# Performance work log

Measured on AMD Instinct MI355X. Metric: run time of the kernel, lower is better.

## Reference

```python
import jax, jax.numpy as jnp
import numpy as np

N_NODES = 50000
N_EDGES = 600000
D_IN = 128
D_HID = 128
D_OUT = 128
LN_EPS = 1e-5


def _layer_norm(h, g, b):
    mu = jnp.mean(h, axis=-1, keepdims=True)
    var = jnp.var(h, axis=-1, keepdims=True)
    return (h - mu) * jax.lax.rsqrt(var + LN_EPS) * g + b


def _gin_conv(x, src, dst, w1, b1, w2, b2):
    # sum-aggregate neighbor messages at destination nodes, eps = 0
    agg = jax.ops.segment_sum(x[src], dst, num_segments=x.shape[0])
    h = x + agg
    h = jax.nn.relu(h @ w1 + b1)
    return h @ w2 + b2


def setup_inputs() -> dict:
    key = jax.random.key(0)
    ks = jax.random.split(key, 20)
    x = jax.random.normal(ks[0], (N_NODES, D_IN), dtype=jnp.float32)
    edge_index = jax.random.randint(ks[1], (2, N_EDGES), 0, N_NODES, dtype=jnp.int64)
    dims = [(D_IN, D_HID), (D_HID, D_HID), (D_HID, D_HID), (D_HID, D_OUT)]
    inp = {"x": x, "edge_index": edge_index}
    for i, (din, dout) in enumerate(dims):
        s1 = 1.0 / np.sqrt(din)
        s2 = 1.0 / np.sqrt(D_HID)
        inp[f"w1_{i}"] = jax.random.uniform(ks[2 + 4 * i], (din, D_HID), jnp.float32, -s1, s1)
        inp[f"b1_{i}"] = jax.random.uniform(ks[3 + 4 * i], (D_HID,), jnp.float32, -s1, s1)
        inp[f"w2_{i}"] = jax.random.uniform(ks[4 + 4 * i], (D_HID, dout), jnp.float32, -s2, s2)
        inp[f"b2_{i}"] = jax.random.uniform(ks[5 + 4 * i], (dout,), jnp.float32, -s2, s2)
    for i in range(3):  # LayerNorm only on first 3 blocks
        inp[f"g_{i}"] = jnp.ones((D_HID,), jnp.float32)
        inp[f"beta_{i}"] = jnp.zeros((D_HID,), jnp.float32)
    return inp


def reference(x, edge_index,
              w1_0, b1_0, w2_0, b2_0,
              w1_1, b1_1, w2_1, b2_1,
              w1_2, b1_2, w2_2, b2_2,
              w1_3, b1_3, w2_3, b2_3,
              g_0, beta_0, g_1, beta_1, g_2, beta_2):
    src, dst = edge_index[0], edge_index[1]
    mlps = [(w1_0, b1_0, w2_0, b2_0), (w1_1, b1_1, w2_1, b2_1),
            (w1_2, b1_2, w2_2, b2_2), (w1_3, b1_3, w2_3, b2_3)]
    lns = [(g_0, beta_0), (g_1, beta_1), (g_2, beta_2)]
    h = x
    for i in range(3):
        h = _gin_conv(h, src, dst, *mlps[i])
        h = _layer_norm(h, *lns[i])
        h = jax.nn.relu(h)  # dropout rate 0.0 -> identity
    h = _gin_conv(h, src, dst, *mlps[3])  # final block: no norm/act
    return h
```

## Files before the change

### kernel.cpp

```cpp
#include <hip/hip_runtime.h>
#include <hip/hip_bf16.h>

#define NN 50000
#define NE 600000
#define DD 128
#define LDSW 136
#define NB 196
#define BSH 8
#define BSTR 4096
#define EPB 2048
#define NBLK_AC ((NE + EPB - 1) / EPB)

typedef __bf16 bf16;
typedef __attribute__((ext_vector_type(8))) __bf16 bf16x8;
typedef __attribute__((ext_vector_type(4))) float f32x4;
typedef __attribute__((ext_vector_type(4))) unsigned int u32x4;
typedef __attribute__((ext_vector_type(4))) unsigned short u16x4;
typedef unsigned short u16;

__device__ __forceinline__ float bf_lo(unsigned int u) {
    return __builtin_bit_cast(float, u << 16);
}
__device__ __forceinline__ float bf_hi(unsigned int u) {
    return __builtin_bit_cast(float, u & 0xffff0000u);
}
__device__ __forceinline__ unsigned int bf_pack(float x, float y) {
    u16 a = __builtin_bit_cast(u16, (bf16)x);
    u16 b = __builtin_bit_cast(u16, (bf16)y);
    return (unsigned int)a | ((unsigned int)b << 16);
}

struct Ptr8 { const float* p[8]; };

__device__ __forceinline__ int edge_dst(const int* ei, int e, int f) {
    return f ? ei[2 * NE + 2 * e] : ei[NE + e];
}
__device__ __forceinline__ int edge_src(const int* ei, int e, int f) {
    return f ? ei[2 * e] : ei[e];
}

#define J1 (NN * DD / 4)
#define J2 (J1 + 8 * DD * DD)

__global__ __launch_bounds__(256) void k_init(const float* __restrict__ x,
                                              u16* __restrict__ xb,
                                              Ptr8 ws, u16* __restrict__ wt,
                                              int* __restrict__ bcnt,
                                              const int* __restrict__ ei,
                                              int* __restrict__ flag) {
    int tid = threadIdx.x;
    if (blockIdx.x == 0) {
        if (tid == 0) flag[0] = 1;
        __syncthreads();
        if (ei[2 * tid + 1] != 0) flag[0] = 0;
    }
    int id = blockIdx.x * 256 + tid;
    if (id < NB) bcnt[id] = 0;
    if (id < J1) {
        f32x4 v = *(const f32x4*)(x + (size_t)id * 4);
        u16x4 o;
        o.x = __builtin_bit_cast(u16, (bf16)v.x);
        o.y = __builtin_bit_cast(u16, (bf16)v.y);
        o.z = __builtin_bit_cast(u16, (bf16)v.z);
        o.w = __builtin_bit_cast(u16, (bf16)v.w);
        *(u16x4*)(xb + (size_t)id * 4) = o;
    } else if (id < J2) {
        int i = id - J1;
        int m = i >> 14;
        int rem = i & 16383;
        int k = rem >> 7;
        int n = rem & 127;
        bf16 b = (bf16)ws.p[m][k * DD + n];
        wt[(size_t)m * DD * DD + n * DD + k] = __builtin_bit_cast(u16, b);
    }
}

__global__ __launch_bounds__(256) void k_scatter(const int* __restrict__ ei,
                                                 const int* __restrict__ flag,
                                                 int* __restrict__ bcnt,
                                                 unsigned int* __restrict__ tmp) {
    __shared__ int lh[NB];
    __shared__ int gb[NB];
    int tid = threadIdx.x;
    if (tid < NB) lh[tid] = 0;
    __syncthreads();
    int f = flag[0];
    int src[8], dst[8], lp[8];
    bool val[8];
#pragma unroll
    for (int k = 0; k < 8; k++) {
        int e = blockIdx.x * EPB + k * 256 + tid;
        val[k] = (e < NE);
        if (val[k]) {
            src[k] = edge_src(ei, e, f);
            dst[k] = edge_dst(ei, e, f);
            lp[k] = atomicAdd(&lh[dst[k] >> BSH], 1);
        }
    }
    __syncthreads();
    if (tid < NB && lh[tid] > 0) gb[tid] = atomicAdd(&bcnt[tid], lh[tid]);
    __syncthreads();
#pragma unroll
    for (int k = 0; k < 8; k++) {
        if (val[k]) {
            int bkt = dst[k] >> BSH;
            unsigned int pk = (unsigned)src[k] | ((unsigned)(dst[k] & 255) << 16);
            tmp[(size_t)bkt * BSTR + gb[bkt] + lp[k]] = pk;
        }
    }
}

__global__ __launch_bounds__(256) void k_build(const unsigned int* __restrict__ tmp,
                                               const int* __restrict__ bcnt,
                                               int* __restrict__ row_start,
                                               int* __restrict__ adj) {
    __shared__ int cnt[256];
    __shared__ int ccur[256];
    __shared__ int sm[4];
    int b = blockIdx.x, tid = threadIdx.x;
    int base = b << BSH;
    int lane = tid & 63, w = tid >> 6;
    cnt[tid] = 0;
    int v = (tid < b) ? bcnt[tid] : 0;
#pragma unroll
    for (int off = 1; off < 64; off <<= 1) v += __shfl_xor(v, off);
    if (lane == 0) sm[w] = v;
    __syncthreads();
    int G = sm[0] + sm[1] + sm[2] + sm[3];
    int n = bcnt[b];
    size_t ts = (size_t)b * BSTR;
    for (int i = tid; i < n; i += 256) {
        atomicAdd(&cnt[tmp[ts + i] >> 16], 1);
    }
    __syncthreads();
    int v2 = cnt[tid];
    int orig = v2;
#pragma unroll
    for (int off = 1; off < 64; off <<= 1) {
        int t = __shfl_up(v2, off);
        if (lane >= off) v2 += t;
    }
    if (lane == 63) sm[w] = v2;
    __syncthreads();
    int add = 0;
    for (int k = 0; k < w; k++) add += sm[k];
    int ex = G + (v2 - orig) + add;
    ccur[tid] = ex;
    if (base + tid < NN) row_start[base + tid] = ex;
    if (b == 0 && tid == 0) row_start[NN] = NE;
    __syncthreads();
    for (int i = tid; i < n; i += 256) {
        unsigned int pk = tmp[ts + i];
        int p = atomicAdd(&ccur[pk >> 16], 1);
        adj[p] = (int)(pk & 0xffffu);
    }
}

__global__ __launch_bounds__(256) void k_agg(const u16* __restrict__ xb,
                                             const int* __restrict__ row_start,
                                             const int* __restrict__ adj,
                                             u16* __restrict__ out) {
    int gid = blockIdx.x * blockDim.x + threadIdx.x;
    int wave = gid >> 6, lane = gid & 63;
    int grp = lane >> 4, l = lane & 15;
    int node = wave * 4 + grp;
    if (node >= NN) return;
    const u32x4* base = (const u32x4*)xb;
    u32x4 sv = base[(size_t)node * 16 + l];
    float af[8], bf[8];
#pragma unroll
    for (int j = 0; j < 4; j++) {
        af[2 * j] = bf_lo(sv[j]); af[2 * j + 1] = bf_hi(sv[j]);
        bf[2 * j] = 0.f; bf[2 * j + 1] = 0.f;
    }
    int s = row_start[node], e = row_start[node + 1];
    int i = s;
    for (; i + 7 < e; i += 8) {
        u32x4 t0 = base[(size_t)adj[i] * 16 + l];
        u32x4 t1 = base[(size_t)adj[i + 1] * 16 + l];
        u32x4 t2 = base[(size_t)adj[i + 2] * 16 + l];
        u32x4 t3 = base[(size_t)adj[i + 3] * 16 + l];
        u32x4 t4 = base[(size_t)adj[i + 4] * 16 + l];
        u32x4 t5 = base[(size_t)adj[i + 5] * 16 + l];
        u32x4 t6 = base[(size_t)adj[i + 6] * 16 + l];
        u32x4 t7 = base[(size_t)adj[i + 7] * 16 + l];
#pragma unroll
        for (int j = 0; j < 4; j++) {
            af[2 * j]     += (bf_lo(t0[j]) + bf_lo(t1[j])) + (bf_lo(t2[j]) + bf_lo(t3[j]));
            af[2 * j + 1] += (bf_hi(t0[j]) + bf_hi(t1[j])) + (bf_hi(t2[j]) + bf_hi(t3[j]));
            bf[2 * j]     += (bf_lo(t4[j]) + bf_lo(t5[j])) + (bf_lo(t6[j]) + bf_lo(t7[j]));
            bf[2 * j + 1] += (bf_hi(t4[j]) + bf_hi(t5[j])) + (bf_hi(t6[j]) + bf_hi(t7[j]));
        }
    }
    for (; i + 3 < e; i += 4) {
        u32x4 t0 = base[(size_t)adj[i] * 16 + l];
        u32x4 t1 = base[(size_t)adj[i + 1] * 16 + l];
        u32x4 t2 = base[(size_t)adj[i + 2] * 16 + l];
        u32x4 t3 = base[(size_t)adj[i + 3] * 16 + l];
#pragma unroll
        for (int j = 0; j < 4; j++) {
            af[2 * j]     += bf_lo(t0[j]) + bf_lo(t1[j]);
            af[2 * j + 1] += bf_hi(t0[j]) + bf_hi(t1[j]);
            bf[2 * j]     += bf_lo(t2[j]) + bf_lo(t3[j]);
            bf[2 * j + 1] += bf_hi(t2[j]) + bf_hi(t3[j]);
        }
    }
    for (; i < e; i++) {
        u32x4 t = base[(size_t)adj[i] * 16 + l];
#pragma unroll
        for (int j = 0; j < 4; j++) { af[2 * j] += bf_lo(t[j]); af[2 * j + 1] += bf_hi(t[j]); }
    }
    u32x4 o;
#pragma unroll
    for (int j = 0; j < 4; j++) o[j] = bf_pack(af[2 * j] + bf[2 * j], af[2 * j + 1] + bf[2 * j + 1]);
    ((u32x4*)out)[(size_t)node * 16 + l] = o;
}

template <bool LN, bool B16OUT>
__global__ __launch_bounds__(64) void k_mlp(const u16* __restrict__ hin,
                                            const u16* __restrict__ w1t,
                                            const float* __restrict__ b1,
                                            const u16* __restrict__ w2t,
                                            const float* __restrict__ b2,
                                            const float* __restrict__ g,
                                            const float* __restrict__ bta,
                                            void* __restrict__ hout) {
    __shared__ u16 lds[64 * LDSW];
    const int lane = threadIdx.x;
    const int l15 = lane & 15, l4 = lane >> 4;
    const int tile0 = blockIdx.x * 64;

#pragma unroll
    for (int it = 0; it < 16; ++it) {
        int slot = lane + it * 64;
        int row = slot >> 4, c16 = slot & 15;
        u32x4 v = {0u, 0u, 0u, 0u};
        int grow = tile0 + row;
        if (grow < NN) v = *(const u32x4*)(hin + (size_t)grow * DD + c16 * 8);
        *(u32x4*)&lds[row * LDSW + c16 * 8] = v;
    }
    __syncthreads();

    float b1c[8], b2c[8], gc[8], bc[8];
#pragma unroll
    for (int c = 0; c < 8; c++) {
        int col = c * 16 + l15;
        b1c[c] = b1[col];
        b2c[c] = b2[col];
        if (LN) { gc[c] = g[col]; bc[c] = bta[col]; }
    }

    f32x4 acc[4][8];
#pragma unroll
    for (int r = 0; r < 4; r++)
#pragma unroll
        for (int c = 0; c < 8; c++) acc[r][c] = (f32x4){0.f, 0.f, 0.f, 0.f};

#pragma unroll
    for (int ks = 0; ks < 4; ++ks) {
        bf16x8 a0 = __builtin_bit_cast(bf16x8,
            *(const u32x4*)&lds[(l15) * LDSW + ks * 32 + l4 * 8]);
        bf16x8 a1 = __builtin_bit_cast(bf16x8,
            *(const u32x4*)&lds[(16 + l15) * LDSW + ks * 32 + l4 * 8]);
        bf16x8 a2 = __builtin_bit_cast(bf16x8,
            *(const u32x4*)&lds[(32 + l15) * LDSW + ks * 32 + l4 * 8]);
        bf16x8 a3 = __builtin_bit_cast(bf16x8,
            *(const u32x4*)&lds[(48 + l15) * LDSW + ks * 32 + l4 * 8]);
#pragma unroll
        for (int c = 0; c < 8; c++) {
            bf16x8 b = __builtin_bit_cast(bf16x8,
                *(const u32x4*)(w1t + (size_t)(c * 16 + l15) * DD + ks * 32 + l4 * 8));
            acc[0][c] = __builtin_amdgcn_mfma_f32_16x16x32_bf16(a0, b, acc[0][c], 0, 0, 0);
            acc[1][c] = __builtin_amdgcn_mfma_f32_16x16x32_bf16(a1, b, acc[1][c], 0, 0, 0);
            acc[2][c] = __builtin_amdgcn_mfma_f32_16x16x32_bf16(a2, b, acc[2][c], 0, 0, 0);
            acc[3][c] = __builtin_amdgcn_mfma_f32_16x16x32_bf16(a3, b, acc[3][c], 0, 0, 0);
        }
    }

#pragma unroll
    for (int r = 0; r < 4; r++) {
#pragma unroll
        for (int c = 0; c < 8; c++) {
            int col = c * 16 + l15;
#pragma unroll
            for (int j = 0; j < 4; j++) {
                float v = acc[r][c][j] + b1c[c];
                v = v > 0.f ? v : 0.f;
                bf16 b = (bf16)v;
                int row = r * 16 + l4 * 4 + j;
                lds[row * LDSW + col] = __builtin_bit_cast(u16, b);
            }
        }
    }

#pragma unroll
    for (int r = 0; r < 4; r++)
#pragma unroll
        for (int c = 0; c < 8; c++) acc[r][c] = (f32x4){0.f, 0.f, 0.f, 0.f};

#pragma unroll
    for (int ks = 0; ks < 4; ++ks) {
        bf16x8 a0 = __builtin_bit_cast(bf16x8,
            *(const u32x4*)&lds[(l15) * LDSW + ks * 32 + l4 * 8]);
        bf16x8 a1 = __builtin_bit_cast(bf16x8,
            *(const u32x4*)&lds[(16 + l15) * LDSW + ks * 32 + l4 * 8]);
        bf16x8 a2 = __builtin_bit_cast(bf16x8,
            *(const u32x4*)&lds[(32 + l15) * LDSW + ks * 32 + l4 * 8]);
        bf16x8 a3 = __builtin_bit_cast(bf16x8,
            *(const u32x4*)&lds[(48 + l15) * LDSW + ks * 32 + l4 * 8]);
#pragma unroll
        for (int c = 0; c < 8; c++) {
            bf16x8 b = __builtin_bit_cast(bf16x8,
                *(const u32x4*)(w2t + (size_t)(c * 16 + l15) * DD + ks * 32 + l4 * 8));
            acc[0][c] = __builtin_amdgcn_mfma_f32_16x16x32_bf16(a0, b, acc[0][c], 0, 0, 0);
            acc[1][c] = __builtin_amdgcn_mfma_f32_16x16x32_bf16(a1, b, acc[1][c], 0, 0, 0);
            acc[2][c] = __builtin_amdgcn_mfma_f32_16x16x32_bf16(a2, b, acc[2][c], 0, 0, 0);
            acc[3][c] = __builtin_amdgcn_mfma_f32_16x16x32_bf16(a3, b, acc[3][c], 0, 0, 0);
        }
    }

#pragma unroll
    for (int r = 0; r < 4; r++) {
        float vals[8][4];
#pragma unroll
        for (int c = 0; c < 8; c++)
#pragma unroll
            for (int j = 0; j < 4; j++) vals[c][j] = acc[r][c][j] + b2c[c];

        if (LN) {
            float s[4], q[4];
#pragma unroll
            for (int j = 0; j < 4; j++) {
                s[j] = 0.f; q[j] = 0.f;
#pragma unroll
                for (int c = 0; c < 8; c++) {
                    s[j] += vals[c][j];
                    q[j] += vals[c][j] * vals[c][j];
                }
            }
#pragma unroll
            for (int m = 1; m <= 8; m <<= 1) {
#pragma unroll
                for (int j = 0; j < 4; j++) {
                    s[j] += __shfl_xor(s[j], m);
                    q[j] += __shfl_xor(q[j], m);
                }
            }
#pragma unroll
            for (int j = 0; j < 4; j++) {
                float mu = s[j] * (1.f / 128.f);
                float var = q[j] * (1.f / 128.f) - mu * mu;
                float rs = rsqrtf(var + 1e-5f);
#pragma unroll
                for (int c = 0; c < 8; c++) {
                    float v = (vals[c][j] - mu) * rs * gc[c] + bc[c];
                    vals[c][j] = v > 0.f ? v : 0.f;
                }
            }
        }

        if (B16OUT) {
#pragma unroll
            for (int c = 0; c < 8; c++) {
                int col = c * 16 + l15;
#pragma unroll
                for (int j = 0; j < 4; j++) {
                    int row = r * 16 + l4 * 4 + j;
                    lds[row * LDSW + col] =
                        __builtin_bit_cast(u16, (bf16)vals[c][j]);
                }
            }
        } else {
#pragma unroll
            for (int c = 0; c < 8; c++) {
                int col = c * 16 + l15;
#pragma unroll
                for (int j = 0; j < 4; j++) {
                    int row = tile0 + r * 16 + l4 * 4 + j;
                    if (row < NN)
                        ((float*)hout)[(size_t)row * DD + col] = vals[c][j];
                }
            }
        }
    }

    if (B16OUT) {
#pragma unroll
        for (int it = 0; it < 16; ++it) {
            int slot = it * 64 + lane;
            int row = slot >> 4;
            int c16 = slot & 15;
            u32x4 v = *(const u32x4*)&lds[row * LDSW + c16 * 8];
            int grow = tile0 + row;
            if (grow < NN)
                *(u32x4*)((u16*)hout + (size_t)grow * DD + c16 * 8) = v;
        }
    }
}

extern "C" void kernel_launch(void* const* d_in, const int* in_sizes, int n_in,
                              void* d_out, int out_size, void* d_ws, size_t ws_size,
                              hipStream_t stream) {
    const float* x = (const float*)d_in[0];
    const int* ei = (const int*)d_in[1];
    const float* w1[4]; const float* b1[4]; const float* w2[4]; const float* b2[4];
    for (int i = 0; i < 4; i++) {
        w1[i] = (const float*)d_in[2 + 4 * i];
        b1[i] = (const float*)d_in[3 + 4 * i];
        w2[i] = (const float*)d_in[4 + 4 * i];
        b2[i] = (const float*)d_in[5 + 4 * i];
    }
    const float* g[3]; const float* bt[3];
    for (int i = 0; i < 3; i++) {
        g[i] = (const float*)d_in[18 + 2 * i];
        bt[i] = (const float*)d_in[19 + 2 * i];
    }

    char* ws = (char*)d_ws;
    size_t off = 0;
    auto alloc = [&](size_t bytes) -> char* {
        char* p = ws + off;
        off = (off + bytes + 255) & ~(size_t)255;
        return p;
    };
    int* flag          = (int*)alloc(4);
    int* row_start     = (int*)alloc((NN + 1) * 4);
    int* bcnt          = (int*)alloc(NB * 4);
    int* adj           = (int*)alloc(NE * 4);
    unsigned int* tmp  = (unsigned int*)alloc((size_t)NB * BSTR * 4);
    u16* wt            = (u16*)alloc((size_t)8 * DD * DD * 2);
    u16* xb            = (u16*)alloc((size_t)NN * DD * 2);
    u16* hbf           = (u16*)alloc((size_t)NN * DD * 2);
    u16* hA            = (u16*)alloc((size_t)NN * DD * 2);
    u16* hB            = (u16*)alloc((size_t)NN * DD * 2);

    Ptr8 p8;
    for (int i = 0; i < 4; i++) {
        p8.p[2 * i] = w1[i];
        p8.p[2 * i + 1] = w2[i];
    }

    k_init<<<(J2 + 255) / 256, 256, 0, stream>>>(x, xb, p8, wt, bcnt, ei, flag);
    k_scatter<<<NBLK_AC, 256, 0, stream>>>(ei, flag, bcnt, tmp);
    k_build<<<NB, 256, 0, stream>>>(tmp, bcnt, row_start, adj);

    const int mgrid = (NN + 63) / 64;
    const u16* hin = xb;
    for (int i = 0; i < 4; i++) {
        k_agg<<<(NN / 4 * 64) / 256, 256, 0, stream>>>(hin, row_start, adj, hbf);
        const u16* w1ti = wt + (size_t)(2 * i) * DD * DD;
        const u16* w2ti = wt + (size_t)(2 * i + 1) * DD * DD;
        if (i < 3) {
            u16* outp = (i & 1) ? hB : hA;
            k_mlp<true, true><<<mgrid, 64, 0, stream>>>(
                hbf, w1ti, b1[i], w2ti, b2[i], g[i], bt[i], outp);
            hin = outp;
        } else {
            k_mlp<false, false><<<mgrid, 64, 0, stream>>>(
                hbf, w1ti, b1[i], w2ti, b2[i], nullptr, nullptr, d_out);
        }
    }
}
```

Baseline: 229.3 us.

## Split MLP tile rows across two waves per block

The fused MLP kernel now runs 128 threads per block, so each of two wavefronts handles 32 of the 64 rows instead of one wave doing all 64. This halves the per-wave accumulator registers, which should raise occupancy, and doubles the number of waves issuing MFMA work per tile. Each wave reads and writes only its own rows in LDS between the two GEMMs, so no extra barrier is needed. The cost is that each wave loads the full weight fragments on its own, so global/L2 weight traffic per tile doubles.

```diff
diff --git a/kernel.cpp b/kernel.cpp
--- a/kernel.cpp
+++ b/kernel.cpp
@@ -217,22 +217,32 @@
 }
 
 template <bool LN, bool B16OUT>
-__global__ __launch_bounds__(64) void k_mlp(const u16* __restrict__ hin,
-                                            const u16* __restrict__ w1t,
-                                            const float* __restrict__ b1,
-                                            const u16* __restrict__ w2t,
-                                            const float* __restrict__ b2,
-                                            const float* __restrict__ g,
-                                            const float* __restrict__ bta,
-                                            void* __restrict__ hout) {
+__global__ __launch_bounds__(128) void k_mlp(const u16* __restrict__ hin,
+                                             const u16* __restrict__ w1t,
+                                             const float* __restrict__ b1,
+                                             const u16* __restrict__ w2t,
+                                             const float* __restrict__ b2,
+                                             const float* __restrict__ g,
+                                             const float* __restrict__ bta,
+                                             void* __restrict__ hout) {
     __shared__ u16 lds[64 * LDSW];
-    const int lane = threadIdx.x;
+    const int tid = threadIdx.x;
+    const int wv = tid >> 6, lane = tid & 63;
     const int l15 = lane & 15, l4 = lane >> 4;
     const int tile0 = blockIdx.x * 64;
 
-#pragma unroll
-    for (int it = 0; it < 16; ++it) {
-        int slot = lane + it * 64;
+    float b1c[8], b2c[8], gc[8], bc[8];
+#pragma unroll
+    for (int c = 0; c < 8; c++) {
+        int col = c * 16 + l15;
+        b1c[c] = b1[col];
+        b2c[c] = b2[col];
+        if (LN) { gc[c] = g[col]; bc[c] = bta[col]; }
+    }
+
+#pragma unroll
+    for (int it = 0; it < 8; ++it) {
+        int slot = tid + it * 128;
         int row = slot >> 4, c16 = slot & 15;
         u32x4 v = {0u, 0u, 0u, 0u};
         int grow = tile0 + row;
@@ -241,44 +251,31 @@
     }
     __syncthreads();
 
-    float b1c[8], b2c[8], gc[8], bc[8];
-#pragma unroll
-    for (int c = 0; c < 8; c++) {
-        int col = c * 16 + l15;
-        b1c[c] = b1[col];
-        b2c[c] = b2[col];
-        if (LN) { gc[c] = g[col]; bc[c] = bta[col]; }
-    }
-
-    f32x4 acc[4][8];
-#pragma unroll
-    for (int r = 0; r < 4; r++)
+    f32x4 acc[2][8];
+#pragma unroll
+    for (int r = 0; r < 2; r++)
 #pragma unroll
         for (int c = 0; c < 8; c++) acc[r][c] = (f32x4){0.f, 0.f, 0.f, 0.f};
+
+    const int rowbase = wv * 32;
 
 #pragma unroll
     for (int ks = 0; ks < 4; ++ks) {
         bf16x8 a0 = __builtin_bit_cast(bf16x8,
-            *(const u32x4*)&lds[(l15) * LDSW + ks * 32 + l4 * 8]);
+            *(const u32x4*)&lds[(rowbase + l15) * LDSW + ks * 32 + l4 * 8]);
         bf16x8 a1 = __builtin_bit_cast(bf16x8,
-            *(const u32x4*)&lds[(16 + l15) * LDSW + ks * 32 + l4 * 8]);
-        bf16x8 a2 = __builtin_bit_cast(bf16x8,
-            *(const u32x4*)&lds[(32 + l15) * LDSW + ks * 32 + l4 * 8]);
-        bf16x8 a3 = __builtin_bit_cast(bf16x8,
-            *(const u32x4*)&lds[(48 + l15) * LDSW + ks * 32 + l4 * 8]);
+            *(const u32x4*)&lds[(rowbase + 16 + l15) * LDSW + ks * 32 + l4 * 8]);
 #pragma unroll
         for (int c = 0; c < 8; c++) {
             bf16x8 b = __builtin_bit_cast(bf16x8,
                 *(const u32x4*)(w1t + (size_t)(c * 16 + l15) * DD + ks * 32 + l4 * 8));
             acc[0][c] = __builtin_amdgcn_mfma_f32_16x16x32_bf16(a0, b, acc[0][c], 0, 0, 0);
             acc[1][c] = __builtin_amdgcn_mfma_f32_16x16x32_bf16(a1, b, acc[1][c], 0, 0, 0);
-            acc[2][c] = __builtin_amdgcn_mfma_f32_16x16x32_bf16(a2, b, acc[2][c], 0, 0, 0);
-            acc[3][c] = __builtin_amdgcn_mfma_f32_16x16x32_bf16(a3, b, acc[3][c], 0, 0, 0);
-        }
-    }
-
-#pragma unroll
-    for (int r = 0; r < 4; r++) {
+        }
+    }
+
+#pragma unroll
+    for (int r = 0; r < 2; r++) {
 #pragma unroll
         for (int c = 0; c < 8; c++) {
             int col = c * 16 + l15;
@@ -287,40 +284,34 @@
                 float v = acc[r][c][j] + b1c[c];
                 v = v > 0.f ? v : 0.f;
                 bf16 b = (bf16)v;
-                int row = r * 16 + l4 * 4 + j;
+                int row = rowbase + r * 16 + l4 * 4 + j;
                 lds[row * LDSW + col] = __builtin_bit_cast(u16, b);
             }
         }
     }
 
 #pragma unroll
-    for (int r = 0; r < 4; r++)
+    for (int r = 0; r < 2; r++)
 #pragma unroll
         for (int c = 0; c < 8; c++) acc[r][c] = (f32x4){0.f, 0.f, 0.f, 0.f};
 
 #pragma unroll
     for (int ks = 0; ks < 4; ++ks) {
         bf16x8 a0 = __builtin_bit_cast(bf16x8,
-            *(const u32x4*)&lds[(l15) * LDSW + ks * 32 + l4 * 8]);
+            *(const u32x4*)&lds[(rowbase + l15) * LDSW + ks * 32 + l4 * 8]);
         bf16x8 a1 = __builtin_bit_cast(bf16x8,
-            *(const u32x4*)&lds[(16 + l15) * LDSW + ks * 32 + l4 * 8]);
-        bf16x8 a2 = __builtin_bit_cast(bf16x8,
-            *(const u32x4*)&lds[(32 + l15) * LDSW + ks * 32 + l4 * 8]);
-        bf16x8 a3 = __builtin_bit_cast(bf16x8,
-            *(const u32x4*)&lds[(48 + l15) * LDSW + ks * 32 + l4 * 8]);
+            *(const u32x4*)&lds[(rowbase + 16 + l15) * LDSW + ks * 32 + l4 * 8]);
 #pragma unroll
         for (int c = 0; c < 8; c++) {
             bf16x8 b = __builtin_bit_cast(bf16x8,
                 *(const u32x4*)(w2t + (size_t)(c * 16 + l15) * DD + ks * 32 + l4 * 8));
             acc[0][c] = __builtin_amdgcn_mfma_f32_16x16x32_bf16(a0, b, acc[0][c], 0, 0, 0);
             acc[1][c] = __builtin_amdgcn_mfma_f32_16x16x32_bf16(a1, b, acc[1][c], 0, 0, 0);
-            acc[2][c] = __builtin_amdgcn_mfma_f32_16x16x32_bf16(a2, b, acc[2][c], 0, 0, 0);
-            acc[3][c] = __builtin_amdgcn_mfma_f32_16x16x32_bf16(a3, b, acc[3][c], 0, 0, 0);
-        }
-    }
-
-#pragma unroll
-    for (int r = 0; r < 4; r++) {
+        }
+    }
+
+#pragma unroll
+    for (int r = 0; r < 2; r++) {
         float vals[8][4];
 #pragma unroll
         for (int c = 0; c < 8; c++)
@@ -365,7 +356,7 @@
                 int col = c * 16 + l15;
 #pragma unroll
                 for (int j = 0; j < 4; j++) {
-                    int row = r * 16 + l4 * 4 + j;
+                    int row = rowbase + r * 16 + l4 * 4 + j;
                     lds[row * LDSW + col] =
                         __builtin_bit_cast(u16, (bf16)vals[c][j]);
                 }
@@ -376,7 +367,7 @@
                 int col = c * 16 + l15;
 #pragma unroll
                 for (int j = 0; j < 4; j++) {
-                    int row = tile0 + r * 16 + l4 * 4 + j;
+                    int row = tile0 + rowbase + r * 16 + l4 * 4 + j;
                     if (row < NN)
                         ((float*)hout)[(size_t)row * DD + col] = vals[c][j];
                 }
@@ -386,9 +377,9 @@
 
     if (B16OUT) {
 #pragma unroll
-        for (int it = 0; it < 16; ++it) {
+        for (int it = 0; it < 8; ++it) {
             int slot = it * 64 + lane;
-            int row = slot >> 4;
+            int row = rowbase + (slot >> 4);
             int c16 = slot & 15;
             u32x4 v = *(const u32x4*)&lds[row * LDSW + c16 * 8];
             int grow = tile0 + row;
@@ -452,11 +443,11 @@
         const u16* w2ti = wt + (size_t)(2 * i + 1) * DD * DD;
         if (i < 3) {
             u16* outp = (i & 1) ? hB : hA;
-            k_mlp<true, true><<<mgrid, 64, 0, stream>>>(
+            k_mlp<true, true><<<mgrid, 128, 0, stream>>>(
                 hbf, w1ti, b1[i], w2ti, b2[i], g[i], bt[i], outp);
             hin = outp;
         } else {
-            k_mlp<false, false><<<mgrid, 64, 0, stream>>>(
+            k_mlp<false, false><<<mgrid, 128, 0, stream>>>(
                 hbf, w1ti, b1[i], w2ti, b2[i], nullptr, nullptr, d_out);
         }
     }
```

Result: no change. 230.9 us, median of 2 (+0.7%).
